# Performance work log

Hardware: AMD Instinct MI355X
Metric: run time of the kernel (lower is better)

Reference implementation:

```python
import jax, jax.numpy as jnp
import numpy as np

SCORE_THRESH = 0.05
NMS_THRESH = 0.5
MAX_DET = 100
BBOX_XFORM_CLIP = float(np.log(1000.0 / 16.0))


def decode_boxes(proposals, deltas):
    # proposals, deltas: [..., 4] in (x1, y1, x2, y2) / (dx, dy, dw, dh)
    w = proposals[..., 2] - proposals[..., 0]
    h = proposals[..., 3] - proposals[..., 1]
    cx = proposals[..., 0] + 0.5 * w
    cy = proposals[..., 1] + 0.5 * h
    dx, dy = deltas[..., 0], deltas[..., 1]
    dw = jnp.minimum(deltas[..., 2], BBOX_XFORM_CLIP)
    dh = jnp.minimum(deltas[..., 3], BBOX_XFORM_CLIP)
    pcx = dx * w + cx
    pcy = dy * h + cy
    pw = jnp.exp(dw) * w
    ph = jnp.exp(dh) * h
    return jnp.stack([pcx - 0.5 * pw, pcy - 0.5 * ph,
                      pcx + 0.5 * pw, pcy + 0.5 * ph], axis=-1)


def iou_matrix(boxes):
    # boxes: [N, 4] -> [N, N] pairwise IoU
    area = (boxes[:, 2] - boxes[:, 0]) * (boxes[:, 3] - boxes[:, 1])
    lt = jnp.maximum(boxes[:, None, :2], boxes[None, :, :2])
    rb = jnp.minimum(boxes[:, None, 2:], boxes[None, :, 2:])
    wh = jnp.clip(rb - lt, 0.0)
    inter = wh[..., 0] * wh[..., 1]
    union = area[:, None] + area[None, :] - inter
    return inter / (union + 1e-9)


def nms_single(boxes, scores, labels, valid):
    # Greedy batched NMS for one image with fixed shapes.
    N = boxes.shape[0]
    neg = jnp.finfo(scores.dtype).min
    s = jnp.where(valid, scores, neg)
    # class-offset trick (torchvision batched_nms)
    max_coord = jnp.max(jnp.where(valid[:, None], boxes, 0.0))
    obox = boxes + labels.astype(boxes.dtype)[:, None] * (max_coord + 1.0)
    order = jnp.argsort(-s)
    obox_s = obox[order]
    s_s = s[order]
    valid_s = valid[order]
    iou = iou_matrix(obox_s)  # [N, N]
    idxs = jnp.arange(N)

    def body(i, suppressed):
        keep_i = jnp.logical_and(~suppressed[i], valid_s[i])
        return suppressed | (keep_i & (iou[i] > NMS_THRESH) & (idxs > i))

    suppressed = jax.lax.fori_loop(0, N, body, jnp.zeros((N,), bool))
    keep = (~suppressed) & valid_s
    final_s = jnp.where(keep, s_s, neg)
    top_s, top_i = jax.lax.top_k(final_s, MAX_DET)
    sel = order[top_i]
    valid_out = keep[top_i]
    out_boxes = jnp.where(valid_out[:, None], boxes[sel], 0.0)
    out_scores = jnp.where(valid_out, top_s, 0.0)
    out_labels = jnp.where(valid_out, labels[sel], -1)
    return out_boxes, out_scores, out_labels


def setup_inputs() -> dict:
    key = jax.random.key(0)
    k1, k2, k3, k4, k5 = jax.random.split(key, 5)
    B, N, C = 16, 1024, 91
    class_logits = jax.random.normal(k1, (B, N, C), dtype=jnp.float32)
    bbox_deltas = 0.1 * jax.random.normal(k2, (B, N, C * 4), dtype=jnp.float32)
    xy = jax.random.uniform(k3, (B, N, 2), dtype=jnp.float32) * 800.0
    wh = jax.random.uniform(k4, (B, N, 2), dtype=jnp.float32) * 200.0 + 1.0
    roi_proposals = jnp.concatenate([xy, xy + wh], axis=-1)
    image_sizes = jax.random.randint(k5, (B, 2), 512, 1333).astype(jnp.int32)  # (h, w)
    return {"class_logits": class_logits, "bbox_deltas": bbox_deltas,
            "roi_proposals": roi_proposals, "image_sizes": image_sizes}


def reference(class_logits, bbox_deltas, roi_proposals, image_sizes):
    B, N, C = class_logits.shape
    probs_all = jax.nn.softmax(class_logits, axis=-1)
    scores = jnp.max(probs_all, axis=-1)          # [B, N]
    labels = jnp.argmax(probs_all, axis=-1)       # [B, N]
    valid = (labels > 0) & (scores > SCORE_THRESH)
    # gather per-class deltas (same as the 4*idx .. 4*idx+3 gather)
    deltas = bbox_deltas.reshape(B, N, C, 4)
    matched = jnp.take_along_axis(deltas, labels[:, :, None, None], axis=2)[:, :, 0, :]
    boxes = decode_boxes(roi_proposals, matched)
    hw = image_sizes.astype(boxes.dtype)          # (h, w)
    bound = jnp.stack([hw[:, 1], hw[:, 0], hw[:, 1], hw[:, 0]], axis=-1)[:, None, :]
    boxes = jnp.clip(boxes, 0.0, bound)
    out_boxes, out_scores, out_labels = jax.vmap(nms_single)(boxes, scores, labels, valid)
    return out_boxes, out_scores, out_labels
```

## Files before the change

kernel.cpp:

```cpp
#include <hip/hip_runtime.h>
#include <math.h>

#define NN 1024
#define CC 91
#define MAXDET 100
typedef unsigned long long ull;
#define SENT 0xFFFFFFFFFFFFFFFFULL

struct alignas(16) D4 { double x, y, z, w; };

__device__ __forceinline__ double fexp(double x) {
    const double LOG2E = 1.4426950408889634074;
    const double LN2HI = 6.9314718036912381649e-01;
    const double LN2LO = 1.9082149292705877000e-10;
    double y = x * LOG2E;
    double n = rint(y);
    double t = fma(-n, LN2HI, x);
    t = fma(-n, LN2LO, t);
    double p = 1.1470745597729725e-11;
    p = fma(p, t, 1.6059043836821613e-10);
    p = fma(p, t, 2.0876756987868099e-09);
    p = fma(p, t, 2.5052108385441720e-08);
    p = fma(p, t, 2.7557319223985893e-07);
    p = fma(p, t, 2.7557319223985890e-06);
    p = fma(p, t, 2.4801587301587302e-05);
    p = fma(p, t, 1.9841269841269841e-04);
    p = fma(p, t, 1.3888888888888889e-03);
    p = fma(p, t, 8.3333333333333332e-03);
    p = fma(p, t, 4.1666666666666664e-02);
    p = fma(p, t, 1.6666666666666666e-01);
    p = fma(p, t, 0.5);
    p = fma(p, t, 1.0);
    p = fma(p, t, 1.0);
    double r = ldexp(p, (int)n);
    return x < -745.0 ? 0.0 : r;
}

__global__ __launch_bounds__(256) void k1_fused(
    const float* __restrict__ logits, const float* __restrict__ deltas,
    const float* __restrict__ props,  const int* __restrict__ imsz,
    D4* __restrict__ dbox, double* __restrict__ score64,
    int* __restrict__ label, ull* __restrict__ skeyG, ull* __restrict__ keptKey)
{
    __shared__ double sE[4];
    __shared__ int    sI[4];
    int lane = threadIdx.x & 63;
    int wv   = threadIdx.x >> 6;
    int pid  = blockIdx.x * 4 + wv;
    const float* lg = logits + (size_t)pid * CC;

    float v0 = lg[lane];
    float v1 = (lane < CC - 64) ? lg[64 + lane] : -INFINITY;

    float mm = fmaxf(v0, v1);
    #pragma unroll
    for (int off = 32; off > 0; off >>= 1) mm = fmaxf(mm, __shfl_xor(mm, off));
    ull b0 = __ballot(v0 == mm);
    int idx;
    if (b0) idx = __builtin_ctzll(b0);
    else    idx = 64 + __builtin_ctzll(__ballot(v1 == mm));

    double e = fexp((double)v0 - (double)mm) + fexp((double)v1 - (double)mm);
    #pragma unroll
    for (int off = 32; off > 0; off >>= 1) e += __shfl_xor(e, off);

    if (lane == 0) { sE[wv] = e; sI[wv] = idx; }
    __syncthreads();

    int t = threadIdx.x;
    if (t < 4) {
        int pid2 = blockIdx.x * 4 + t;
        double score = 1.0 / sE[t];
        int lbl = sI[t];
        int vld = (lbl > 0 && score > 0.05) ? 1 : 0;
        float4 d = ((const float4*)deltas)[(size_t)pid2 * CC + lbl];
        float4 p = ((const float4*)props)[pid2];
        double w  = (double)p.z - (double)p.x;
        double h  = (double)p.w - (double)p.y;
        double cx = (double)p.x + 0.5 * w;
        double cy = (double)p.y + 0.5 * h;
        const double CLIPV = 4.135166556742356;
        double dw = fmin((double)d.z, CLIPV), dh = fmin((double)d.w, CLIPV);
        double pcx = (double)d.x * w + cx, pcy = (double)d.y * h + cy;
        double pw = exp(dw) * w, ph = exp(dh) * h;
        double x1 = pcx - 0.5 * pw, y1 = pcy - 0.5 * ph;
        double x2 = pcx + 0.5 * pw, y2 = pcy + 0.5 * ph;
        int b = pid2 >> 10;
        double bw = (double)imsz[b * 2 + 1], bh = (double)imsz[b * 2 + 0];
        x1 = fmin(fmax(x1, 0.0), bw); y1 = fmin(fmax(y1, 0.0), bh);
        x2 = fmin(fmax(x2, 0.0), bw); y2 = fmin(fmax(y2, 0.0), bh);
        dbox[pid2]    = D4{x1, y1, x2, y2};
        score64[pid2] = score;
        label[pid2]   = vld ? lbl : 0;
        double seff = vld ? score : -1e300;
        ull u   = (ull)__double_as_longlong(seff);
        ull asc = (u >> 63) ? ~u : (u | 0x8000000000000000ULL);
        skeyG[pid2]   = (~asc & ~1023ULL) | (ull)(pid2 & 1023);
        keptKey[pid2] = SENT;
    }
}

__global__ __launch_bounds__(256) void k2_nms(
    const D4* __restrict__ dbox, const int* __restrict__ label,
    const ull* __restrict__ skeyG, ull* __restrict__ keptKey)
{
    __shared__ int sMemb[4 * 64];
    __shared__ int sPosR[4 * 64];
    __shared__ ull sKeyR[4 * 64];
    int lane = threadIdx.x & 63, wv = threadIdx.x >> 6;
    int gw = blockIdx.x * 4 + wv;
    int b  = gw / 90;
    int c  = 1 + gw % 90;
    int base = b * NN;
    ull lmlt = (lane == 0) ? 0ULL : ((1ULL << lane) - 1ULL);

    int myl[16];
    #pragma unroll
    for (int w = 0; w < 16; ++w) myl[w] = label[base + w * 64 + lane];

    int nmem = 0;
    #pragma unroll
    for (int w = 0; w < 16; ++w) {
        bool match = (myl[w] == c);
        ull mb = __ballot(match);
        if (match) {
            int slot = nmem + (int)__popcll(mb & lmlt);
            if (slot < 64) sMemb[wv * 64 + slot] = w * 64 + lane;
        }
        nmem += (int)__popcll(mb);
        if (nmem >= 64) break;
    }
    int n = nmem < 64 ? nmem : 64;
    if (n == 0) return;

    int p = sMemb[wv * 64 + (lane < n ? lane : 0)];
    ull key = skeyG[base + p];
    int rank = 0;
    for (int j = 0; j < n; ++j) {
        ull kj = __shfl(key, j);
        rank += (int)(kj < key);
    }
    if (lane < n) { sPosR[wv * 64 + rank] = p; sKeyR[wv * 64 + rank] = key; }
    int rl  = wv * 64 + (lane < n ? lane : 0);
    int p2  = sPosR[rl];
    ull k2v = sKeyR[rl];

    D4 bx = dbox[base + p2];
    double ma = (bx.z - bx.x) * (bx.w - bx.y);
    ull pm = 0;
    for (int j = 0; j < n; ++j) {
        double jx = __shfl(bx.x, j), jy = __shfl(bx.y, j);
        double jz = __shfl(bx.z, j), jw = __shfl(bx.w, j);
        double ja = __shfl(ma, j);
        double xx1 = fmax(bx.x, jx), yy1 = fmax(bx.y, jy);
        double xx2 = fmin(bx.z, jz), yy2 = fmin(bx.w, jw);
        double iw = fmax(xx2 - xx1, 0.0), ih = fmax(yy2 - yy1, 0.0);
        double inter = iw * ih;
        bool hit = (inter > 0.5 * (ma + ja - inter + 1e-9)) && (j < lane);
        pm |= ((ull)hit) << j;
    }
    bool act = lane < n;
    ull avail = __ballot(act);
    ull keptw = 0; bool supp = false;
    while (avail) {
        int k0 = __builtin_ctzll(avail);
        keptw |= 1ULL << k0;
        supp = supp || ((pm >> k0) & 1ULL);
        avail &= ~__ballot(supp);
        avail &= ~((2ULL << k0) - 1ULL);
    }
    if (act && ((keptw >> lane) & 1ULL)) keptKey[base + p2] = k2v;
}

__global__ __launch_bounds__(1024) void k3_top(
    const D4* __restrict__ dbox, const double* __restrict__ score64,
    const int* __restrict__ label, const ull* __restrict__ keptKey,
    float* __restrict__ out)
{
    __shared__ ull sRun[NN];
    int b = blockIdx.x, t = threadIdx.x;
    int lane = t & 63, wv = t >> 6;
    int base = b * NN;

    ull key = keptKey[base + t];
    for (int k = 2; k <= 64; k <<= 1)
        for (int j = k >> 1; j > 0; j >>= 1) {
            ull part = __shfl_xor(key, j);
            bool keepMin = ((lane & j) == 0) == ((lane & k) == 0);
            ull mn = key < part ? key : part;
            ull mx = key < part ? part : key;
            key = keepMin ? mn : mx;
        }
    sRun[wv * 64 + lane] = key;
    __syncthreads();

    if (wv < 8) {
        ull a  = sRun[wv * 128 + lane];
        ull bb = sRun[wv * 128 + 64 + lane];
        ull br = __shfl(bb, 63 - lane);
        ull lo = a < br ? a : br;
        ull hi = a < br ? br : a;
        #pragma unroll
        for (int j = 32; j > 0; j >>= 1) {
            bool km = ((lane & j) == 0);
            ull pl = __shfl_xor(lo, j);
            lo = km ? (lo < pl ? lo : pl) : (lo < pl ? pl : lo);
            ull ph = __shfl_xor(hi, j);
            hi = km ? (hi < ph ? hi : ph) : (hi < ph ? ph : hi);
        }
        sRun[wv * 128 + lane] = lo;
        sRun[wv * 128 + 64 + lane] = hi;
    }
    for (int nm = 4; nm >= 1; nm >>= 1) {
        __syncthreads();
        ull Alo = 0, Ahi = 0, Blo = 0, Bhi = 0;
        if (wv < nm) {
            Alo = sRun[wv * 256 + lane];
            Ahi = sRun[wv * 256 + 64 + lane];
            Blo = sRun[wv * 256 + 128 + lane];
            Bhi = sRun[wv * 256 + 192 + lane];
        }
        __syncthreads();
        if (wv < nm) {
            ull rBhi = __shfl(Bhi, 63 - lane);
            ull rBlo = __shfl(Blo, 63 - lane);
            ull Mlo = Alo < rBhi ? Alo : rBhi;
            ull Mhi = Ahi < rBlo ? Ahi : rBlo;
            ull l2 = Mlo < Mhi ? Mlo : Mhi;
            ull h2 = Mlo < Mhi ? Mhi : Mlo;
            #pragma unroll
            for (int j = 32; j > 0; j >>= 1) {
                bool km = ((lane & j) == 0);
                ull pl = __shfl_xor(l2, j);
                l2 = km ? (l2 < pl ? l2 : pl) : (l2 < pl ? pl : l2);
                ull ph = __shfl_xor(h2, j);
                h2 = km ? (h2 < ph ? h2 : ph) : (h2 < ph ? ph : h2);
            }
            sRun[wv * 128 + lane] = l2;
            sRun[wv * 128 + 64 + lane] = h2;
        }
    }
    if (wv == 0) {
        float* oBox   = out;
        float* oScore = out + 6400;
        float* oLabel = out + 8000;
        #pragma unroll
        for (int rsel = 0; rsel < 2; ++rsel) {
            int rank = rsel * 64 + lane;
            if (rank < MAXDET) {
                ull kf = sRun[rsel * 64 + lane];
                int q = b * MAXDET + rank;
                if (kf == SENT) {
                    oBox[q * 4 + 0] = 0.f; oBox[q * 4 + 1] = 0.f;
                    oBox[q * 4 + 2] = 0.f; oBox[q * 4 + 3] = 0.f;
                    oScore[q] = 0.f;
                    oLabel[q] = -1.f;
                } else {
                    int p = (int)(kf & 1023ULL);
                    D4 bx = dbox[base + p];
                    oBox[q * 4 + 0] = (float)bx.x; oBox[q * 4 + 1] = (float)bx.y;
                    oBox[q * 4 + 2] = (float)bx.z; oBox[q * 4 + 3] = (float)bx.w;
                    oScore[q] = (float)score64[base + p];
                    oLabel[q] = (float)label[base + p];
                }
            }
        }
    }
}

extern "C" void kernel_launch(void* const* d_in, const int* in_sizes, int n_in,
                              void* d_out, int out_size, void* d_ws, size_t ws_size,
                              hipStream_t stream) {
    const float* logits = (const float*)d_in[0];
    const float* deltas = (const float*)d_in[1];
    const float* props  = (const float*)d_in[2];
    const int*   imsz   = (const int*)d_in[3];
    char* ws = (char*)d_ws;
    D4*     dbox    = (D4*)(ws + 0);
    double* score64 = (double*)(ws + 524288);
    int*    label   = (int*)(ws + 655360);
    ull*    skeyG   = (ull*)(ws + 720896);
    ull*    keptKey = (ull*)(ws + 851968);
    float*  out     = (float*)d_out;

    k1_fused<<<dim3(4096), dim3(256), 0, stream>>>(logits, deltas, props, imsz,
                                                   dbox, score64, label, skeyG, keptKey);
    k2_nms<<<dim3(360), dim3(256), 0, stream>>>(dbox, label, skeyG, keptKey);
    k3_top<<<dim3(16), dim3(1024), 0, stream>>>(dbox, score64, label, keptKey, out);
}
```

Before: 94.95 us.

## Fuse NMS and top-k kernels using per-image atomic completion counters

Merges the per-class NMS kernel and the per-image top-k kernel into one launch. The first 90 blocks of 1024 threads run NMS with 16 waves each, and each wave bumps a per-image counter when it finishes. The remaining 16 blocks spin on that counter before sorting and writing output. This removes one kernel launch and the gap between kernels. It relies on all blocks being co-resident, so the spin-wait could deadlock if the consumer blocks are scheduled before the producers, and it adds atomic polling and fences.

After: 152.4 us. +60.5%, slower.

```diff
diff --git a/kernel.cpp b/kernel.cpp
--- a/kernel.cpp
+++ b/kernel.cpp
@@ -40,10 +40,12 @@
     const float* __restrict__ logits, const float* __restrict__ deltas,
     const float* __restrict__ props,  const int* __restrict__ imsz,
     D4* __restrict__ dbox, double* __restrict__ score64,
-    int* __restrict__ label, ull* __restrict__ skeyG, ull* __restrict__ keptKey)
+    int* __restrict__ label, ull* __restrict__ skeyG, ull* __restrict__ keptKey,
+    int* __restrict__ cnt)
 {
     __shared__ double sE[4];
     __shared__ int    sI[4];
+    if (blockIdx.x == 0 && threadIdx.x < 16) cnt[threadIdx.x] = 0;
     int lane = threadIdx.x & 63;
     int wv   = threadIdx.x >> 6;
     int pid  = blockIdx.x * 4 + wv;
@@ -100,168 +102,173 @@
     }
 }
 
-__global__ __launch_bounds__(256) void k2_nms(
-    const D4* __restrict__ dbox, const int* __restrict__ label,
-    const ull* __restrict__ skeyG, ull* __restrict__ keptKey)
-{
-    __shared__ int sMemb[4 * 64];
-    __shared__ int sPosR[4 * 64];
-    __shared__ ull sKeyR[4 * 64];
-    int lane = threadIdx.x & 63, wv = threadIdx.x >> 6;
-    int gw = blockIdx.x * 4 + wv;
-    int b  = gw / 90;
-    int c  = 1 + gw % 90;
-    int base = b * NN;
-    ull lmlt = (lane == 0) ? 0ULL : ((1ULL << lane) - 1ULL);
-
-    int myl[16];
-    #pragma unroll
-    for (int w = 0; w < 16; ++w) myl[w] = label[base + w * 64 + lane];
-
-    int nmem = 0;
-    #pragma unroll
-    for (int w = 0; w < 16; ++w) {
-        bool match = (myl[w] == c);
-        ull mb = __ballot(match);
-        if (match) {
-            int slot = nmem + (int)__popcll(mb & lmlt);
-            if (slot < 64) sMemb[wv * 64 + slot] = w * 64 + lane;
-        }
-        nmem += (int)__popcll(mb);
-        if (nmem >= 64) break;
-    }
-    int n = nmem < 64 ? nmem : 64;
-    if (n == 0) return;
-
-    int p = sMemb[wv * 64 + (lane < n ? lane : 0)];
-    ull key = skeyG[base + p];
-    int rank = 0;
-    for (int j = 0; j < n; ++j) {
-        ull kj = __shfl(key, j);
-        rank += (int)(kj < key);
-    }
-    if (lane < n) { sPosR[wv * 64 + rank] = p; sKeyR[wv * 64 + rank] = key; }
-    int rl  = wv * 64 + (lane < n ? lane : 0);
-    int p2  = sPosR[rl];
-    ull k2v = sKeyR[rl];
-
-    D4 bx = dbox[base + p2];
-    double ma = (bx.z - bx.x) * (bx.w - bx.y);
-    ull pm = 0;
-    for (int j = 0; j < n; ++j) {
-        double jx = __shfl(bx.x, j), jy = __shfl(bx.y, j);
-        double jz = __shfl(bx.z, j), jw = __shfl(bx.w, j);
-        double ja = __shfl(ma, j);
-        double xx1 = fmax(bx.x, jx), yy1 = fmax(bx.y, jy);
-        double xx2 = fmin(bx.z, jz), yy2 = fmin(bx.w, jw);
-        double iw = fmax(xx2 - xx1, 0.0), ih = fmax(yy2 - yy1, 0.0);
-        double inter = iw * ih;
-        bool hit = (inter > 0.5 * (ma + ja - inter + 1e-9)) && (j < lane);
-        pm |= ((ull)hit) << j;
-    }
-    bool act = lane < n;
-    ull avail = __ballot(act);
-    ull keptw = 0; bool supp = false;
-    while (avail) {
-        int k0 = __builtin_ctzll(avail);
-        keptw |= 1ULL << k0;
-        supp = supp || ((pm >> k0) & 1ULL);
-        avail &= ~__ballot(supp);
-        avail &= ~((2ULL << k0) - 1ULL);
-    }
-    if (act && ((keptw >> lane) & 1ULL)) keptKey[base + p2] = k2v;
-}
-
-__global__ __launch_bounds__(1024) void k3_top(
+__global__ __launch_bounds__(1024) void k23_fused(
     const D4* __restrict__ dbox, const double* __restrict__ score64,
-    const int* __restrict__ label, const ull* __restrict__ keptKey,
+    const int* __restrict__ label, const ull* __restrict__ skeyG,
+    ull* __restrict__ keptKey, int* __restrict__ cnt,
     float* __restrict__ out)
 {
+    __shared__ int sMemb[16 * 64];
+    __shared__ int sPosR[16 * 64];
+    __shared__ ull sKeyR[16 * 64];
     __shared__ ull sRun[NN];
-    int b = blockIdx.x, t = threadIdx.x;
-    int lane = t & 63, wv = t >> 6;
-    int base = b * NN;
-
-    ull key = keptKey[base + t];
-    for (int k = 2; k <= 64; k <<= 1)
-        for (int j = k >> 1; j > 0; j >>= 1) {
-            ull part = __shfl_xor(key, j);
-            bool keepMin = ((lane & j) == 0) == ((lane & k) == 0);
-            ull mn = key < part ? key : part;
-            ull mx = key < part ? part : key;
-            key = keepMin ? mn : mx;
-        }
-    sRun[wv * 64 + lane] = key;
-    __syncthreads();
-
-    if (wv < 8) {
-        ull a  = sRun[wv * 128 + lane];
-        ull bb = sRun[wv * 128 + 64 + lane];
-        ull br = __shfl(bb, 63 - lane);
-        ull lo = a < br ? a : br;
-        ull hi = a < br ? br : a;
+    int t = threadIdx.x, lane = t & 63, wv = t >> 6;
+
+    if (blockIdx.x < 90) {
+        int gw = blockIdx.x * 16 + wv;
+        int b  = gw / 90;
+        int c  = 1 + gw % 90;
+        int base = b * NN;
+        ull lmlt = (lane == 0) ? 0ULL : ((1ULL << lane) - 1ULL);
+
+        int myl[16];
         #pragma unroll
-        for (int j = 32; j > 0; j >>= 1) {
-            bool km = ((lane & j) == 0);
-            ull pl = __shfl_xor(lo, j);
-            lo = km ? (lo < pl ? lo : pl) : (lo < pl ? pl : lo);
-            ull ph = __shfl_xor(hi, j);
-            hi = km ? (hi < ph ? hi : ph) : (hi < ph ? ph : hi);
-        }
-        sRun[wv * 128 + lane] = lo;
-        sRun[wv * 128 + 64 + lane] = hi;
-    }
-    for (int nm = 4; nm >= 1; nm >>= 1) {
+        for (int w = 0; w < 16; ++w) myl[w] = label[base + w * 64 + lane];
+
+        int nmem = 0;
+        #pragma unroll
+        for (int w = 0; w < 16; ++w) {
+            bool match = (myl[w] == c);
+            ull mb = __ballot(match);
+            if (match) {
+                int slot = nmem + (int)__popcll(mb & lmlt);
+                if (slot < 64) sMemb[wv * 64 + slot] = w * 64 + lane;
+            }
+            nmem += (int)__popcll(mb);
+            if (nmem >= 64) break;
+        }
+        int n = nmem < 64 ? nmem : 64;
+        if (n > 0) {
+            int p = sMemb[wv * 64 + (lane < n ? lane : 0)];
+            ull key = skeyG[base + p];
+            int rank = 0;
+            for (int j = 0; j < n; ++j) {
+                ull kj = __shfl(key, j);
+                rank += (int)(kj < key);
+            }
+            if (lane < n) { sPosR[wv * 64 + rank] = p; sKeyR[wv * 64 + rank] = key; }
+            int rl  = wv * 64 + (lane < n ? lane : 0);
+            int p2  = sPosR[rl];
+            ull k2v = sKeyR[rl];
+
+            D4 bx = dbox[base + p2];
+            double ma = (bx.z - bx.x) * (bx.w - bx.y);
+            ull pm = 0;
+            for (int j = 0; j < n; ++j) {
+                double jx = __shfl(bx.x, j), jy = __shfl(bx.y, j);
+                double jz = __shfl(bx.z, j), jw = __shfl(bx.w, j);
+                double ja = __shfl(ma, j);
+                double xx1 = fmax(bx.x, jx), yy1 = fmax(bx.y, jy);
+                double xx2 = fmin(bx.z, jz), yy2 = fmin(bx.w, jw);
+                double iw = fmax(xx2 - xx1, 0.0), ih = fmax(yy2 - yy1, 0.0);
+                double inter = iw * ih;
+                bool hit = (inter > 0.5 * (ma + ja - inter + 1e-9)) && (j < lane);
+                pm |= ((ull)hit) << j;
+            }
+            bool act = lane < n;
+            ull avail = __ballot(act);
+            ull keptw = 0; bool supp = false;
+            while (avail) {
+                int k0 = __builtin_ctzll(avail);
+                keptw |= 1ULL << k0;
+                supp = supp || ((pm >> k0) & 1ULL);
+                avail &= ~__ballot(supp);
+                avail &= ~((2ULL << k0) - 1ULL);
+            }
+            if (act && ((keptw >> lane) & 1ULL)) keptKey[base + p2] = k2v;
+        }
+        __threadfence();
+        if (lane == 0) atomicAdd(&cnt[b], 1);
+    } else {
+        int b = blockIdx.x - 90;
+        int base = b * NN;
+        if (t == 0) {
+            while (atomicAdd(&cnt[b], 0) != 90) { __builtin_amdgcn_s_sleep(8); }
+        }
         __syncthreads();
-        ull Alo = 0, Ahi = 0, Blo = 0, Bhi = 0;
-        if (wv < nm) {
-            Alo = sRun[wv * 256 + lane];
-            Ahi = sRun[wv * 256 + 64 + lane];
-            Blo = sRun[wv * 256 + 128 + lane];
-            Bhi = sRun[wv * 256 + 192 + lane];
-        }
+        __threadfence();
+
+        ull key = keptKey[base + t];
+        for (int k = 2; k <= 64; k <<= 1)
+            for (int j = k >> 1; j > 0; j >>= 1) {
+                ull part = __shfl_xor(key, j);
+                bool keepMin = ((lane & j) == 0) == ((lane & k) == 0);
+                ull mn = key < part ? key : part;
+                ull mx = key < part ? part : key;
+                key = keepMin ? mn : mx;
+            }
+        sRun[wv * 64 + lane] = key;
         __syncthreads();
-        if (wv < nm) {
-            ull rBhi = __shfl(Bhi, 63 - lane);
-            ull rBlo = __shfl(Blo, 63 - lane);
-            ull Mlo = Alo < rBhi ? Alo : rBhi;
-            ull Mhi = Ahi < rBlo ? Ahi : rBlo;
-            ull l2 = Mlo < Mhi ? Mlo : Mhi;
-            ull h2 = Mlo < Mhi ? Mhi : Mlo;
+
+        if (wv < 8) {
+            ull a  = sRun[wv * 128 + lane];
+            ull bb = sRun[wv * 128 + 64 + lane];
+            ull br = __shfl(bb, 63 - lane);
+            ull lo = a < br ? a : br;
+            ull hi = a < br ? br : a;
             #pragma unroll
             for (int j = 32; j > 0; j >>= 1) {
                 bool km = ((lane & j) == 0);
-                ull pl = __shfl_xor(l2, j);
-                l2 = km ? (l2 < pl ? l2 : pl) : (l2 < pl ? pl : l2);
-                ull ph = __shfl_xor(h2, j);
-                h2 = km ? (h2 < ph ? h2 : ph) : (h2 < ph ? ph : h2);
-            }
-            sRun[wv * 128 + lane] = l2;
-            sRun[wv * 128 + 64 + lane] = h2;
-        }
-    }
-    if (wv == 0) {
-        float* oBox   = out;
-        float* oScore = out + 6400;
-        float* oLabel = out + 8000;
-        #pragma unroll
-        for (int rsel = 0; rsel < 2; ++rsel) {
-            int rank = rsel * 64 + lane;
-            if (rank < MAXDET) {
-                ull kf = sRun[rsel * 64 + lane];
-                int q = b * MAXDET + rank;
-                if (kf == SENT) {
-                    oBox[q * 4 + 0] = 0.f; oBox[q * 4 + 1] = 0.f;
-                    oBox[q * 4 + 2] = 0.f; oBox[q * 4 + 3] = 0.f;
-                    oScore[q] = 0.f;
-                    oLabel[q] = -1.f;
-                } else {
-                    int p = (int)(kf & 1023ULL);
-                    D4 bx = dbox[base + p];
-                    oBox[q * 4 + 0] = (float)bx.x; oBox[q * 4 + 1] = (float)bx.y;
-                    oBox[q * 4 + 2] = (float)bx.z; oBox[q * 4 + 3] = (float)bx.w;
-                    oScore[q] = (float)score64[base + p];
-                    oLabel[q] = (float)label[base + p];
+                ull pl = __shfl_xor(lo, j);
+                lo = km ? (lo < pl ? lo : pl) : (lo < pl ? pl : lo);
+                ull ph = __shfl_xor(hi, j);
+                hi = km ? (hi < ph ? hi : ph) : (hi < ph ? ph : hi);
+            }
+            sRun[wv * 128 + lane] = lo;
+            sRun[wv * 128 + 64 + lane] = hi;
+        }
+        for (int nm = 4; nm >= 1; nm >>= 1) {
+            __syncthreads();
+            ull Alo = 0, Ahi = 0, Blo = 0, Bhi = 0;
+            if (wv < nm) {
+                Alo = sRun[wv * 256 + lane];
+                Ahi = sRun[wv * 256 + 64 + lane];
+                Blo = sRun[wv * 256 + 128 + lane];
+                Bhi = sRun[wv * 256 + 192 + lane];
+            }
+            __syncthreads();
+            if (wv < nm) {
+                ull rBhi = __shfl(Bhi, 63 - lane);
+                ull rBlo = __shfl(Blo, 63 - lane);
+                ull Mlo = Alo < rBhi ? Alo : rBhi;
+                ull Mhi = Ahi < rBlo ? Ahi : rBlo;
+                ull l2 = Mlo < Mhi ? Mlo : Mhi;
+                ull h2 = Mlo < Mhi ? Mhi : Mlo;
+                #pragma unroll
+                for (int j = 32; j > 0; j >>= 1) {
+                    bool km = ((lane & j) == 0);
+                    ull pl = __shfl_xor(l2, j);
+                    l2 = km ? (l2 < pl ? l2 : pl) : (l2 < pl ? pl : l2);
+                    ull ph = __shfl_xor(h2, j);
+                    h2 = km ? (h2 < ph ? h2 : ph) : (h2 < ph ? ph : h2);
+                }
+                sRun[wv * 128 + lane] = l2;
+                sRun[wv * 128 + 64 + lane] = h2;
+            }
+        }
+        if (wv == 0) {
+            float* oBox   = out;
+            float* oScore = out + 6400;
+            float* oLabel = out + 8000;
+            #pragma unroll
+            for (int rsel = 0; rsel < 2; ++rsel) {
+                int rank = rsel * 64 + lane;
+                if (rank < MAXDET) {
+                    ull kf = sRun[rsel * 64 + lane];
+                    int q = b * MAXDET + rank;
+                    if (kf == SENT) {
+                        oBox[q * 4 + 0] = 0.f; oBox[q * 4 + 1] = 0.f;
+                        oBox[q * 4 + 2] = 0.f; oBox[q * 4 + 3] = 0.f;
+                        oScore[q] = 0.f;
+                        oLabel[q] = -1.f;
+                    } else {
+                        int p = (int)(kf & 1023ULL);
+                        D4 bx = dbox[base + p];
+                        oBox[q * 4 + 0] = (float)bx.x; oBox[q * 4 + 1] = (float)bx.y;
+                        oBox[q * 4 + 2] = (float)bx.z; oBox[q * 4 + 3] = (float)bx.w;
+                        oScore[q] = (float)score64[base + p];
+                        oLabel[q] = (float)label[base + p];
+                    }
                 }
             }
         }
@@ -281,10 +288,12 @@
     int*    label   = (int*)(ws + 655360);
     ull*    skeyG   = (ull*)(ws + 720896);
     ull*    keptKey = (ull*)(ws + 851968);
+    int*    cnt     = (int*)(ws + 983040);
     float*  out     = (float*)d_out;
 
     k1_fused<<<dim3(4096), dim3(256), 0, stream>>>(logits, deltas, props, imsz,
-                                                   dbox, score64, label, skeyG, keptKey);
-    k2_nms<<<dim3(360), dim3(256), 0, stream>>>(dbox, label, skeyG, keptKey);
-    k3_top<<<dim3(16), dim3(1024), 0, stream>>>(dbox, score64, label, keptKey, out);
-}
+                                                   dbox, score64, label, skeyG,
+                                                   keptKey, cnt);
+    k23_fused<<<dim3(106), dim3(1024), 0, stream>>>(dbox, score64, label, skeyG,
+                                                    keptKey, cnt, out);
+}
```
